# Kernel tuning notes

Measured on AMD Instinct MI355X. Metric: run time of the kernel, lower is better.

Reference implementation:

```python
import jax, jax.numpy as jnp
import numpy as np

B, N, DEG, F_IN, D = 32, 1024, 16, 8, 64

def setup_inputs() -> dict:
    key = jax.random.key(0)
    ks = jax.random.split(key, 24)
    T = B * N
    E = B * N * DEG
    x = jax.random.normal(ks[0], (T, F_IN), dtype=jnp.float32)
    # edges confined within each graph (block-diagonal batched graph)
    off = (jnp.arange(B) * N)[:, None]
    src = jax.random.randint(ks[1], (B, N * DEG), 0, N) + off
    dst = jax.random.randint(ks[2], (B, N * DEG), 0, N) + off
    edge_index = jnp.stack([src.reshape(-1), dst.reshape(-1)]).astype(jnp.int64)
    reachable = jax.random.randint(ks[3], (T,), 0, 2, dtype=jnp.int32)
    s = 0.1
    p = lambda k, shp: jax.random.normal(k, shp, dtype=jnp.float32) * s
    return {
        'x': x, 'edge_index': edge_index, 'reachable': reachable,
        'Wl0': p(ks[4], (D, F_IN)), 'Wr0': p(ks[5], (D, F_IN)),
        'att0': p(ks[6], (D,)), 'b0': p(ks[7], (D,)),
        'Wl': p(ks[8], (4, D, D)), 'Wr': p(ks[9], (4, D, D)),
        'att': p(ks[10], (4, D)), 'b': p(ks[11], (4, D)),
        't6w': p(ks[12], (D, D)), 't6b': p(ks[13], (D,)),
        't7w': p(ks[14], (D, D)), 't7b': p(ks[15], (D,)),
        't5pw': p(ks[16], (1, 2 * D)), 't5pb': p(ks[17], (1,)),
        't5vw': p(ks[18], (1, 2 * D)), 't5vb': p(ks[19], (1,)),
        'pw': p(ks[20], (1, 1)), 'pb': p(ks[21], (1,)),
        'vw': p(ks[22], (1, 1)), 'vb': p(ks[23], (1,)),
        'n_per_graph': N,
    }

def reference(x, edge_index, reachable, Wl0, Wr0, att0, b0, Wl, Wr, att, b,
              t6w, t6b, t7w, t7b, t5pw, t5pb, t5vw, t5vb, pw, pb, vw, vb,
              n_per_graph):
    T = x.shape[0]
    n = int(n_per_graph)
    bsz = T // n
    d = Wl0.shape[0]
    # GATv2Conv adds self loops by default
    loop = jnp.arange(T)
    src = jnp.concatenate([edge_index[0], loop])
    dst = jnp.concatenate([edge_index[1], loop])

    def gatv2(h, WlK, WrK, a, bb):
        xl = h @ WlK.T                                  # [T, d]
        xr = h @ WrK.T
        e = jax.nn.leaky_relu(xl[src] + xr[dst], 0.2) @ a  # [E]
        emax = jax.ops.segment_max(e, dst, num_segments=T)
        ee = jnp.exp(e - emax[dst])
        denom = jax.ops.segment_sum(ee, dst, num_segments=T)
        alpha = ee / denom[dst]                         # edge softmax per target
        return jax.ops.segment_sum(alpha[:, None] * xl[src], dst, num_segments=T) + bb

    h = gatv2(x, Wl0, Wr0, att0, b0)
    for k in range(Wl.shape[0]):  # ReLU between layers, none after last
        h = gatv2(jax.nn.relu(h), Wl[k], Wr[k], att[k], b[k])
    mu_raw = h                                          # [T, d]

    # scatter_mean pooling per graph + repeat_interleave back to nodes
    mu_mp = mu_raw.reshape(bsz, n, d).mean(axis=1)      # [B, d]
    mu_mp_exp = jnp.repeat(mu_mp, n, axis=0)            # [T, d]

    g = mu_mp_exp @ t6w.T + t6b
    l = mu_raw @ t7w.T + t7b
    rep = jax.nn.relu(jnp.concatenate([g, l], axis=1))  # [T, 2d]

    prob_logits = rep @ t5pw.T + t5pb                   # [T, 1]
    logits = (prob_logits * pw[0, 0] + pb[0]).reshape(bsz, n, 1)

    q = (rep @ t5vw.T + t5vb)[:, 0]                     # [T]
    q = jnp.where(reachable.astype(bool), q, jnp.float32(-1e20))
    v = q.reshape(bsz, n).max(axis=1, keepdims=True)    # [B, 1]
    value = v * vw[0, 0] + vb[0]
    return logits, value
```

## Files before the change

kernel.cpp:

```cpp
#include <hip/hip_runtime.h>
#include <hip/hip_bf16.h>

typedef unsigned short u16;

#define T_NODES 32768
#define NPG 1024
#define BGR 32
#define D 64
#define FIN 8
#define SLOTS 64

typedef __attribute__((ext_vector_type(8))) short short8v;
typedef __attribute__((ext_vector_type(4))) float floatx4;
typedef __attribute__((ext_vector_type(2))) float f32x2;

__device__ __forceinline__ float bf2f(u16 u){ return __uint_as_float(((unsigned)u) << 16); }
__device__ __forceinline__ u16 f2bf(float f){
    __hip_bfloat16 h = __float2bfloat16(f);
    return *reinterpret_cast<u16*>(&h);
}
__device__ __forceinline__ f32x2 lo_hi(unsigned w){
    f32x2 r;
    r[0] = __uint_as_float(w << 16);
    r[1] = __uint_as_float(w & 0xffff0000u);
    return r;
}
__device__ __forceinline__ f32x2 lrelu2(f32x2 v){
    return __builtin_elementwise_max(v, v * 0.2f);
}
__device__ __forceinline__ short8v pack_bf8(float4 a, float4 b){
    short8v r;
    r[0]=(short)f2bf(a.x); r[1]=(short)f2bf(a.y);
    r[2]=(short)f2bf(a.z); r[3]=(short)f2bf(a.w);
    r[4]=(short)f2bf(b.x); r[5]=(short)f2bf(b.y);
    r[6]=(short)f2bf(b.z); r[7]=(short)f2bf(b.w);
    return r;
}

__device__ __forceinline__ unsigned fenc(float f){
    unsigned b = __float_as_uint(f);
    return (b & 0x80000000u) ? ~b : (b | 0x80000000u);
}
__device__ __forceinline__ float fdec(unsigned k){
    unsigned b = (k & 0x80000000u) ? (k ^ 0x80000000u) : ~k;
    return __uint_as_float(b);
}

template<int CTRL, int RM, int BM>
__device__ __forceinline__ float dpp_add(float x){
    int y = __builtin_amdgcn_update_dpp(0, __float_as_int(x), CTRL, RM, BM, false);
    return x + __int_as_float(y);
}
__device__ __forceinline__ float wave_sum63(float x){
    x = dpp_add<0x111,0xf,0xf>(x);
    x = dpp_add<0x112,0xf,0xf>(x);
    x = dpp_add<0x114,0xf,0xe>(x);
    x = dpp_add<0x118,0xf,0xc>(x);
    x = dpp_add<0x142,0xa,0xf>(x);
    x = dpp_add<0x143,0xc,0xf>(x);
    return x;
}
__device__ __forceinline__ float wave_sum_bcast(float x){
    return __int_as_float(__builtin_amdgcn_readlane(__float_as_int(wave_sum63(x)), 63));
}
__device__ __forceinline__ float row_ror_add(float x){
    x = dpp_add<0x121,0xf,0xf>(x);
    x = dpp_add<0x122,0xf,0xf>(x);
    x = dpp_add<0x124,0xf,0xf>(x);
    x = dpp_add<0x128,0xf,0xf>(x);
    return x;
}

__device__ __forceinline__ void edge_body(uint2 uv, bool valid,
        f32x2 a01, f32x2 a23, f32x2 xr01, f32x2 xr23,
        f32x2& acc01, f32x2& acc23, float& l){
    f32x2 x01 = lo_hi(uv.x);
    f32x2 x23 = lo_hi(uv.y);
    f32x2 v01 = lrelu2(x01 + xr01);
    f32x2 v23 = lrelu2(x23 + xr23);
    f32x2 e2 = v01 * a01 + v23 * a23;
    float e = e2[0] + e2[1];
    e = row_ror_add(e);
    float q = valid ? __expf(e) : 0.f;
    acc01 += q * x01;
    acc23 += q * x23;
    l += q;
}

__device__ __forceinline__ void node_edge(const u16* __restrict__ xlin,
        const int* colSh, int eb, int t, int deg, int sub4,
        f32x2 a01, f32x2 a23, f32x2 xr01, f32x2 xr23,
        f32x2& acc01, f32x2& acc23, float& l){
    int nEdge = deg + 1;
    for (int j0 = 0; j0 < nEdge; j0 += 8){
        uint2 u[8];
        #pragma unroll
        for (int i = 0; i < 8; i++){
            int j = j0 + i;
            int jc = (j < nEdge) ? j : (nEdge-1);
            int s = (jc < deg) ? colSh[eb + jc] : t;
            u[i] = *(const uint2*)&xlin[((size_t)(unsigned)s << 6) + sub4];
        }
        #pragma unroll
        for (int i = 0; i < 8; i++)
            edge_body(u[i], j0 + i < nEdge, a01, a23, xr01, xr23, acc01, acc23, l);
    }
}

__device__ __forceinline__ void el_phase(
        const u16* __restrict__ xlin, const u16* __restrict__ xrin,
        const float* __restrict__ att, const float* __restrict__ bias,
        const float* __restrict__ Wl, const float* __restrict__ Wr,
        u16* __restrict__ xlout, u16* __restrict__ xrout,
        int tid, int rowBase, u16 (*hs)[80], const int* colSh, const int* cnt){
    int wave = tid >> 6, lane = tid & 63;
    int g = lane >> 4, sub4 = (lane & 15) << 2;
    int ln = wave*4 + g;
    int t  = rowBase + ln;
    f32x2 a01 = { att[sub4],   att[sub4+1] };
    f32x2 a23 = { att[sub4+2], att[sub4+3] };
    float4 b4 = *(const float4*)&bias[sub4];
    uint2 xru = *(const uint2*)&xrin[((size_t)t << 6) + sub4];
    f32x2 xr01 = lo_hi(xru.x), xr23 = lo_hi(xru.y);
    int deg = cnt[ln]; deg = deg < SLOTS ? deg : SLOTS;
    f32x2 acc01 = {0.f,0.f}, acc23 = {0.f,0.f};
    float l = 0.f;
    node_edge(xlin, colSh, ln*SLOTS, t, deg, sub4,
              a01, a23, xr01, xr23, acc01, acc23, l);
    float rl = __frcp_rn(l);
    ushort4 hb;
    hb.x = f2bf(fmaxf(fmaf(acc01[0], rl, b4.x), 0.f));
    hb.y = f2bf(fmaxf(fmaf(acc01[1], rl, b4.y), 0.f));
    hb.z = f2bf(fmaxf(fmaf(acc23[0], rl, b4.z), 0.f));
    hb.w = f2bf(fmaxf(fmaf(acc23[1], rl, b4.w), 0.f));
    *(ushort4*)&hs[ln][sub4] = hb;
    int lw = lane & 15, lg = lane >> 4, kb = lg*8;
    int colw = (wave << 4) + lw;
    const float* wl0 = &Wl[colw*D + kb];
    const float* wr0 = &Wr[colw*D + kb];
    short8v bl0 = pack_bf8(*(const float4*)wl0,        *(const float4*)(wl0+4));
    short8v bl1 = pack_bf8(*(const float4*)(wl0+32),   *(const float4*)(wl0+36));
    short8v br0 = pack_bf8(*(const float4*)wr0,        *(const float4*)(wr0+4));
    short8v br1 = pack_bf8(*(const float4*)(wr0+32),   *(const float4*)(wr0+36));
    __syncthreads();
    short8v a0 = *(const short8v*)&hs[lw][kb];
    short8v a1 = *(const short8v*)&hs[lw][32 + kb];
    floatx4 cl = {0.f,0.f,0.f,0.f}, cr = {0.f,0.f,0.f,0.f};
    cl = __builtin_amdgcn_mfma_f32_16x16x32_bf16(a0, bl0, cl, 0, 0, 0);
    cl = __builtin_amdgcn_mfma_f32_16x16x32_bf16(a1, bl1, cl, 0, 0, 0);
    cr = __builtin_amdgcn_mfma_f32_16x16x32_bf16(a0, br0, cr, 0, 0, 0);
    cr = __builtin_amdgcn_mfma_f32_16x16x32_bf16(a1, br1, cr, 0, 0, 0);
    size_t rb = (size_t)(rowBase + lg*4);
    #pragma unroll
    for (int j = 0; j < 4; j++){
        xlout[(rb + j)*D + colw] = f2bf(cl[j]);
        xrout[(rb + j)*D + colw] = f2bf(cr[j]);
    }
}

__global__ void lin0_kernel(const float* __restrict__ x, const float* __restrict__ Wl0,
                            const float* __restrict__ Wr0,
                            u16* __restrict__ xlb, u16* __restrict__ xrb,
                            float* __restrict__ muAcc,
                            unsigned* __restrict__ vslot, int* __restrict__ done,
                            int* __restrict__ pgdone, int* __restrict__ pgflag){
    __shared__ float wl[D][FIN+1];
    __shared__ float wr[D][FIN+1];
    __shared__ float xs[32][FIN];
    int tid = threadIdx.x;
    int blk = blockIdx.x;
    int gidx = blk*256 + tid;
    if (gidx < BGR*D)   muAcc[gidx] = 0.f;
    if (gidx < BGR){ vslot[gidx] = 0u; done[gidx] = 0; pgdone[gidx] = 0; pgflag[gidx] = 0; }
    int rowBase = (blk & 7)*4096 + (blk >> 3)*32;
    for (int i = tid; i < D*FIN; i += 256){
        wl[i>>3][i&7] = Wl0[i];
        wr[i>>3][i&7] = Wr0[i];
    }
    xs[tid>>3][tid&7] = x[rowBase*FIN + tid];
    __syncthreads();
    int wave = tid >> 6, lane = tid & 63;
    int rb = rowBase + wave*8;
    #pragma unroll
    for (int r = 0; r < 8; r++){
        float al = 0.f, ar = 0.f;
        int lr = wave*8 + r;
        #pragma unroll
        for (int k = 0; k < FIN; k++){
            float xv = xs[lr][k];
            al = fmaf(xv, wl[lane][k], al);
            ar = fmaf(xv, wr[lane][k], ar);
        }
        xlb[(size_t)(rb+r)*D + lane] = f2bf(al);
        xrb[(size_t)(rb+r)*D + lane] = f2bf(ar);
    }
}

__global__ __launch_bounds__(256) void el0_kernel(
        const int* __restrict__ esrc, const int* __restrict__ edst, int epg,
        const u16* __restrict__ xlin, const u16* __restrict__ xrin,
        const float* __restrict__ att, const float* __restrict__ bias,
        int* __restrict__ counts, int* __restrict__ col64,
        const float* __restrict__ Wl, const float* __restrict__ Wr,
        u16* __restrict__ xlout, u16* __restrict__ xrout){
    __shared__ __align__(16) u16 hs[16][80];
    __shared__ __align__(16) int colSh[16*SLOTS];
    __shared__ int cntL[16];
    int tid = threadIdx.x, blk = blockIdx.x;
    int rowBase = (blk & 7)*4096 + (blk >> 3)*16;
    int g = rowBase >> 10;
    if (tid < 16) cntL[tid] = 0;
    __syncthreads();
    size_t eg0 = (size_t)g * epg;
    const int4* d4 = (const int4*)(edst + eg0);
    const int4* s4 = (const int4*)(esrc + eg0);
    int q4 = epg >> 2;
    for (int i = tid; i < q4; i += 256){
        int4 dv = d4[i];
        int4 sv = s4[i];
        int r;
        r = dv.x - rowBase; if ((unsigned)r < 16u){ int sl = atomicAdd(&cntL[r], 1); if (sl < SLOTS) colSh[(r<<6)+sl] = sv.x; }
        r = dv.y - rowBase; if ((unsigned)r < 16u){ int sl = atomicAdd(&cntL[r], 1); if (sl < SLOTS) colSh[(r<<6)+sl] = sv.y; }
        r = dv.z - rowBase; if ((unsigned)r < 16u){ int sl = atomicAdd(&cntL[r], 1); if (sl < SLOTS) colSh[(r<<6)+sl] = sv.z; }
        r = dv.w - rowBase; if ((unsigned)r < 16u){ int sl = atomicAdd(&cntL[r], 1); if (sl < SLOTS) colSh[(r<<6)+sl] = sv.w; }
    }
    __syncthreads();
    if (tid < 16) counts[rowBase + tid] = cntL[tid];
    *(int4*)&col64[((size_t)rowBase << 6) + tid*4] = *(const int4*)&colSh[tid*4];
    el_phase(xlin, xrin, att, bias, Wl, Wr, xlout, xrout,
             tid, rowBase, hs, colSh, cntL);
}

__global__ __launch_bounds__(256) void el_kernel(
        const u16* __restrict__ xlin, const u16* __restrict__ xrin,
        const float* __restrict__ att, const float* __restrict__ bias,
        const int* __restrict__ counts, const int* __restrict__ col64,
        const float* __restrict__ Wl, const float* __restrict__ Wr,
        u16* __restrict__ xlout, u16* __restrict__ xrout){
    __shared__ __align__(16) u16 hs[16][80];
    __shared__ __align__(16) int colSh[16*SLOTS];
    __shared__ int cnt[16];
    int tid = threadIdx.x, blk = blockIdx.x;
    int rowBase = (blk & 7)*4096 + (blk >> 3)*16;
    if (tid < 16) cnt[tid] = counts[rowBase + tid];
    *(int4*)&colSh[tid*4] = *(const int4*)&col64[((size_t)rowBase << 6) + tid*4];
    __syncthreads();
    el_phase(xlin, xrin, att, bias, Wl, Wr, xlout, xrout,
             tid, rowBase, hs, colSh, cnt);
}

__global__ __launch_bounds__(256) void e4final_kernel(
        const u16* __restrict__ xlin, const u16* __restrict__ xrin,
        const float* __restrict__ att, const float* __restrict__ bias,
        const int* __restrict__ counts, const int* __restrict__ col64,
        const float* __restrict__ t6w, const float* __restrict__ t6b,
        const float* __restrict__ t7w, const float* __restrict__ t7b,
        const float* __restrict__ t5pw, const float* __restrict__ t5pb,
        const float* __restrict__ t5vw, const float* __restrict__ t5vb,
        const float* __restrict__ pw, const float* __restrict__ pb,
        const float* __restrict__ vw, const float* __restrict__ vb,
        const int* __restrict__ reachable,
        float* __restrict__ muAcc, unsigned* __restrict__ vslot,
        int* __restrict__ done, int* __restrict__ pgdone,
        int* __restrict__ pgflag, float* __restrict__ gPQ,
        float* __restrict__ out_logits, float* __restrict__ out_value){
    __shared__ __align__(16) char arena[43776];
    __shared__ float muS[D];
    __shared__ float PgQgS[2];
    __shared__ int isLastS;
    float* hfin  = (float*)arena;
    int*   colSh = (int*)  (arena + 17408);
    int*   cnt   = (int*)  (arena + 33792);
    float* wsH   = (float*)(arena + 17408);
    float* ppar  = (float*)(arena + 34816);
    float* qpar  = (float*)(arena + 39168);

    int tid = threadIdx.x, blk = blockIdx.x;
    int rowBase = (blk & 7)*4096 + (blk >> 3)*64;
    int b = rowBase >> 10;
    if (tid < 64){
        int c = counts[rowBase + tid];
        cnt[tid] = c < SLOTS ? c : SLOTS;
    }
    for (int i = tid; i < 1024; i += 256)
        *(int4*)&colSh[i*4] = *(const int4*)&col64[((size_t)rowBase << 6) + i*4];
    __syncthreads();
    int wave = tid >> 6, lane = tid & 63;
    int g = lane >> 4, sub4 = (lane & 15) << 2;
    int gid = wave*4 + g;
    f32x2 a01 = { att[sub4],   att[sub4+1] };
    f32x2 a23 = { att[sub4+2], att[sub4+3] };
    float4 b4 = *(const float4*)&bias[sub4];
    for (int n = 0; n < 4; n++){
        int ln = gid + n*16;
        int t  = rowBase + ln;
        uint2 xru = *(const uint2*)&xrin[((size_t)t << 6) + sub4];
        f32x2 xr01 = lo_hi(xru.x), xr23 = lo_hi(xru.y);
        int deg = cnt[ln];
        f32x2 acc01 = {0.f,0.f}, acc23 = {0.f,0.f};
        float l = 0.f;
        node_edge(xlin, colSh, ln*SLOTS, t, deg, sub4,
                  a01, a23, xr01, xr23, acc01, acc23, l);
        float rl = __frcp_rn(l);
        float4 hv;
        hv.x = fmaf(acc01[0], rl, b4.x);
        hv.y = fmaf(acc01[1], rl, b4.y);
        hv.z = fmaf(acc23[0], rl, b4.z);
        hv.w = fmaf(acc23[1], rl, b4.w);
        *(float4*)&hfin[ln*68 + sub4] = hv;
    }
    __syncthreads();
    for (int i = tid; i < D*D; i += 256) wsH[(i>>6)*68 + (i&63)] = t7w[i];
    if (wave == 0){
        float s = 0.f;
        #pragma unroll
        for (int nn = 0; nn < 64; nn++) s += hfin[nn*68 + lane];
        atomicAdd(&muAcc[b*D + lane], s);
    }
    __syncthreads();
    if (tid == 0){
        int tk = atomicAdd(&pgdone[b], 1);
        isLastS = (tk == (NPG/64) - 1);
    }
    __syncthreads();
    if (isLastS){
        if (tid < D)
            muS[tid] = __hip_atomic_load(&muAcc[b*D + tid], __ATOMIC_RELAXED,
                                         __HIP_MEMORY_SCOPE_AGENT) * (1.f/NPG);
        __syncthreads();
        if (tid < D){
            int d = tid;
            float gg = t6b[d];
            #pragma unroll
            for (int k = 0; k < D; k++) gg = fmaf(muS[k], t6w[d*D + k], gg);
            gg = fmaxf(gg, 0.f);
            float pp = wave_sum_bcast(gg * t5pw[d]);
            float qq = wave_sum_bcast(gg * t5vw[d]);
            if (d == 0){
                __hip_atomic_store(&gPQ[b*2],   pp, __ATOMIC_RELAXED, __HIP_MEMORY_SCOPE_AGENT);
                __hip_atomic_store(&gPQ[b*2+1], qq, __ATOMIC_RELAXED, __HIP_MEMORY_SCOPE_AGENT);
                asm volatile("s_waitcnt vmcnt(0)" ::: "memory");
                __hip_atomic_store(&pgflag[b], 1, __ATOMIC_RELAXED, __HIP_MEMORY_SCOPE_AGENT);
            }
        }
    }
    int ty = tid >> 4, tx = tid & 15;
    int r0 = ty * 4;
    float acc[4][4];
    #pragma unroll
    for (int i = 0; i < 4; i++)
        #pragma unroll
        for (int j = 0; j < 4; j++) acc[i][j] = 0.f;
    for (int k = 0; k < D; k += 4){
        float4 hv[4], wv[4];
        #pragma unroll
        for (int i = 0; i < 4; i++){
            hv[i] = *(const float4*)&hfin[(r0+i)*68 + k];
            wv[i] = *(const float4*)&wsH[(tx + 16*i)*68 + k];
        }
        #pragma unroll
        for (int i = 0; i < 4; i++)
            #pragma unroll
            for (int j = 0; j < 4; j++)
                acc[i][j] += hv[i].x*wv[j].x + hv[i].y*wv[j].y
                           + hv[i].z*wv[j].z + hv[i].w*wv[j].w;
    }
    float bc[4], pwc[4], qwc[4];
    #pragma unroll
    for (int j = 0; j < 4; j++){
        int c = tx + 16*j;
        bc[j]  = t7b[c];
        pwc[j] = t5pw[D + c];
        qwc[j] = t5vw[D + c];
    }
    #pragma unroll
    for (int i = 0; i < 4; i++){
        float sp = 0.f, sq = 0.f;
        #pragma unroll
        for (int j = 0; j < 4; j++){
            float lv = fmaxf(acc[i][j] + bc[j], 0.f);
            sp = fmaf(lv, pwc[j], sp);
            sq = fmaf(lv, qwc[j], sq);
        }
        ppar[(r0+i)*17 + tx] = sp;
        qpar[(r0+i)*17 + tx] = sq;
    }
    __syncthreads();
    if (tid == 0){
        while (__hip_atomic_load(&pgflag[b], __ATOMIC_RELAXED,
                                 __HIP_MEMORY_SCOPE_AGENT) == 0)
            __builtin_amdgcn_s_sleep(16);
        PgQgS[0] = __hip_atomic_load(&gPQ[b*2],   __ATOMIC_RELAXED, __HIP_MEMORY_SCOPE_AGENT);
        PgQgS[1] = __hip_atomic_load(&gPQ[b*2+1], __ATOMIC_RELAXED, __HIP_MEMORY_SCOPE_AGENT);
    }
    __syncthreads();
    if (tid < 64){
        int t = rowBase + tid;
        float sp = 0.f, sq = 0.f;
        #pragma unroll
        for (int c = 0; c < 16; c++){ sp += ppar[tid*17 + c]; sq += qpar[tid*17 + c]; }
        float prob = PgQgS[0] + sp + t5pb[0];
        out_logits[t] = prob * pw[0] + pb[0];
        float q = PgQgS[1] + sq + t5vb[0];
        if (!reachable[t]) q = -1e20f;
        float m = q;
        #pragma unroll
        for (int o = 1; o < 64; o <<= 1) m = fmaxf(m, __shfl_xor(m, o, 64));
        if (tid == 0){
            atomicMax(&vslot[b], fenc(m));
            asm volatile("s_waitcnt vmcnt(0)" ::: "memory");
            int ticket = atomicAdd(&done[b], 1);
            if (ticket == (NPG/64) - 1){
                unsigned k = __hip_atomic_load(&vslot[b], __ATOMIC_RELAXED,
                                               __HIP_MEMORY_SCOPE_AGENT);
                out_value[b] = fdec(k)*vw[0] + vb[0];
            }
        }
    }
}

extern "C" void kernel_launch(void* const* d_in, const int* in_sizes, int n_in,
                              void* d_out, int out_size, void* d_ws, size_t ws_size,
                              hipStream_t stream){
    const float* x          = (const float*)d_in[0];
    const int*   edge_index = (const int*)d_in[1];
    const int*   reachable  = (const int*)d_in[2];
    const float* Wl0 = (const float*)d_in[3];
    const float* Wr0 = (const float*)d_in[4];
    const float* att0= (const float*)d_in[5];
    const float* b0  = (const float*)d_in[6];
    const float* Wl  = (const float*)d_in[7];
    const float* Wr  = (const float*)d_in[8];
    const float* att = (const float*)d_in[9];
    const float* bb  = (const float*)d_in[10];
    const float* t6w = (const float*)d_in[11];
    const float* t6b = (const float*)d_in[12];
    const float* t7w = (const float*)d_in[13];
    const float* t7b = (const float*)d_in[14];
    const float* t5pw= (const float*)d_in[15];
    const float* t5pb= (const float*)d_in[16];
    const float* t5vw= (const float*)d_in[17];
    const float* t5vb= (const float*)d_in[18];
    const float* pw  = (const float*)d_in[19];
    const float* pb  = (const float*)d_in[20];
    const float* vw  = (const float*)d_in[21];
    const float* vb  = (const float*)d_in[22];

    int E = in_sizes[1] / 2;
    int epg = E / BGR;
    const int* esrc = edge_index;
    const int* edst = edge_index + E;

    char* ws = (char*)d_ws;
    u16* xlbA   = (u16*)ws;
    u16* xrbA   = xlbA + (size_t)T_NODES*D;
    u16* xlbB   = xrbA + (size_t)T_NODES*D;
    u16* xrbB   = xlbB + (size_t)T_NODES*D;
    int* counts = (int*)(xrbB + (size_t)T_NODES*D);
    int* col64  = counts + T_NODES + 16;
    float* muAcc= (float*)(col64 + (size_t)T_NODES*SLOTS);
    unsigned* vslot = (unsigned*)(muAcc + BGR*D);
    int* done   = (int*)(vslot + BGR);
    int* pgdone = done + BGR;
    int* pgflag = pgdone + BGR;
    float* gPQ  = (float*)(pgflag + BGR);

    lin0_kernel<<<T_NODES/32, 256, 0, stream>>>(x, Wl0, Wr0, xlbA, xrbA,
                                                muAcc, vslot, done, pgdone, pgflag);

    el0_kernel<<<T_NODES/16, 256, 0, stream>>>(esrc, edst, epg, xlbA, xrbA, att0, b0,
                                               counts, col64,
                                               Wl + 0*D*D, Wr + 0*D*D, xlbB, xrbB);
    el_kernel<<<T_NODES/16, 256, 0, stream>>>(xlbB, xrbB, att + 0*D, bb + 0*D, counts, col64,
                                              Wl + 1*D*D, Wr + 1*D*D, xlbA, xrbA);
    el_kernel<<<T_NODES/16, 256, 0, stream>>>(xlbA, xrbA, att + 1*D, bb + 1*D, counts, col64,
                                              Wl + 2*D*D, Wr + 2*D*D, xlbB, xrbB);
    el_kernel<<<T_NODES/16, 256, 0, stream>>>(xlbB, xrbB, att + 2*D, bb + 2*D, counts, col64,
                                              Wl + 3*D*D, Wr + 3*D*D, xlbA, xrbA);

    e4final_kernel<<<T_NODES/64, 256, 0, stream>>>(xlbA, xrbA, att + 3*D, bb + 3*D,
                                                   counts, col64, t6w, t6b, t7w, t7b,
                                                   t5pw, t5pb, t5vw, t5vb, pw, pb, vw, vb,
                                                   reachable, muAcc, vslot, done,
                                                   pgdone, pgflag, gPQ,
                                                   (float*)d_out, (float*)d_out + T_NODES);
}
```

Before: 223.3 us.

## Compress adjacency to 16-bit local indices, pre-convert weights, fuse xr0 into el0

Neighbor lists are now stored as u16 offsets relative to the graph base instead of 32-bit global ids, halving adjacency traffic in every layer. The per-layer weights are converted to bf16 once in lin0 instead of being packed from fp32 in every block. The first layer's xr projection is computed on the fly inside el0 from x and Wr0 rather than written and re-read from global memory. This relies on graphs having at most 65536 nodes and adds some redundant small FMA work in el0.

```diff
diff --git a/kernel.cpp b/kernel.cpp
--- a/kernel.cpp
+++ b/kernel.cpp
@@ -27,14 +27,6 @@
 }
 __device__ __forceinline__ f32x2 lrelu2(f32x2 v){
     return __builtin_elementwise_max(v, v * 0.2f);
-}
-__device__ __forceinline__ short8v pack_bf8(float4 a, float4 b){
-    short8v r;
-    r[0]=(short)f2bf(a.x); r[1]=(short)f2bf(a.y);
-    r[2]=(short)f2bf(a.z); r[3]=(short)f2bf(a.w);
-    r[4]=(short)f2bf(b.x); r[5]=(short)f2bf(b.y);
-    r[6]=(short)f2bf(b.z); r[7]=(short)f2bf(b.w);
-    return r;
 }
 
 __device__ __forceinline__ unsigned fenc(float f){
@@ -88,7 +80,7 @@
 }
 
 __device__ __forceinline__ void node_edge(const u16* __restrict__ xlin,
-        const int* colSh, int eb, int t, int deg, int sub4,
+        const u16* colSh, int eb, int gbase, int t, int deg, int sub4,
         f32x2 a01, f32x2 a23, f32x2 xr01, f32x2 xr23,
         f32x2& acc01, f32x2& acc23, float& l){
     int nEdge = deg + 1;
@@ -98,7 +90,7 @@
         for (int i = 0; i < 8; i++){
             int j = j0 + i;
             int jc = (j < nEdge) ? j : (nEdge-1);
-            int s = (jc < deg) ? colSh[eb + jc] : t;
+            int s = (jc < deg) ? (gbase + (int)colSh[eb + jc]) : t;
             u[i] = *(const uint2*)&xlin[((size_t)(unsigned)s << 6) + sub4];
         }
         #pragma unroll
@@ -108,24 +100,24 @@
 }
 
 __device__ __forceinline__ void el_phase(
-        const u16* __restrict__ xlin, const u16* __restrict__ xrin,
+        const u16* __restrict__ xlin,
         const float* __restrict__ att, const float* __restrict__ bias,
-        const float* __restrict__ Wl, const float* __restrict__ Wr,
+        const u16* __restrict__ Wlb, const u16* __restrict__ Wrb,
         u16* __restrict__ xlout, u16* __restrict__ xrout,
-        int tid, int rowBase, u16 (*hs)[80], const int* colSh, const int* cnt){
+        int tid, int rowBase, u16 (*hs)[80], const u16* colSh, const int* cnt,
+        f32x2 xr01, f32x2 xr23){
     int wave = tid >> 6, lane = tid & 63;
     int g = lane >> 4, sub4 = (lane & 15) << 2;
     int ln = wave*4 + g;
     int t  = rowBase + ln;
+    int gbase = (rowBase >> 10) << 10;
     f32x2 a01 = { att[sub4],   att[sub4+1] };
     f32x2 a23 = { att[sub4+2], att[sub4+3] };
     float4 b4 = *(const float4*)&bias[sub4];
-    uint2 xru = *(const uint2*)&xrin[((size_t)t << 6) + sub4];
-    f32x2 xr01 = lo_hi(xru.x), xr23 = lo_hi(xru.y);
     int deg = cnt[ln]; deg = deg < SLOTS ? deg : SLOTS;
     f32x2 acc01 = {0.f,0.f}, acc23 = {0.f,0.f};
     float l = 0.f;
-    node_edge(xlin, colSh, ln*SLOTS, t, deg, sub4,
+    node_edge(xlin, colSh, ln*SLOTS, gbase, t, deg, sub4,
               a01, a23, xr01, xr23, acc01, acc23, l);
     float rl = __frcp_rn(l);
     ushort4 hb;
@@ -136,12 +128,12 @@
     *(ushort4*)&hs[ln][sub4] = hb;
     int lw = lane & 15, lg = lane >> 4, kb = lg*8;
     int colw = (wave << 4) + lw;
-    const float* wl0 = &Wl[colw*D + kb];
-    const float* wr0 = &Wr[colw*D + kb];
-    short8v bl0 = pack_bf8(*(const float4*)wl0,        *(const float4*)(wl0+4));
-    short8v bl1 = pack_bf8(*(const float4*)(wl0+32),   *(const float4*)(wl0+36));
-    short8v br0 = pack_bf8(*(const float4*)wr0,        *(const float4*)(wr0+4));
-    short8v br1 = pack_bf8(*(const float4*)(wr0+32),   *(const float4*)(wr0+36));
+    const u16* wlp = &Wlb[colw*D + kb];
+    const u16* wrp = &Wrb[colw*D + kb];
+    short8v bl0 = *(const short8v*)wlp;
+    short8v bl1 = *(const short8v*)(wlp + 32);
+    short8v br0 = *(const short8v*)wrp;
+    short8v br1 = *(const short8v*)(wrp + 32);
     __syncthreads();
     short8v a0 = *(const short8v*)&hs[lw][kb];
     short8v a1 = *(const short8v*)&hs[lw][32 + kb];
@@ -159,59 +151,67 @@
 }
 
 __global__ void lin0_kernel(const float* __restrict__ x, const float* __restrict__ Wl0,
-                            const float* __restrict__ Wr0,
-                            u16* __restrict__ xlb, u16* __restrict__ xrb,
+                            const float* __restrict__ Wl, const float* __restrict__ Wr,
+                            u16* __restrict__ xlb,
+                            u16* __restrict__ Wlb, u16* __restrict__ Wrb,
                             float* __restrict__ muAcc,
                             unsigned* __restrict__ vslot, int* __restrict__ done,
                             int* __restrict__ pgdone, int* __restrict__ pgflag){
     __shared__ float wl[D][FIN+1];
-    __shared__ float wr[D][FIN+1];
     __shared__ float xs[32][FIN];
     int tid = threadIdx.x;
     int blk = blockIdx.x;
     int gidx = blk*256 + tid;
     if (gidx < BGR*D)   muAcc[gidx] = 0.f;
     if (gidx < BGR){ vslot[gidx] = 0u; done[gidx] = 0; pgdone[gidx] = 0; pgflag[gidx] = 0; }
+    if (gidx < 4*D*D){
+        Wlb[gidx] = f2bf(Wl[gidx]);
+        Wrb[gidx] = f2bf(Wr[gidx]);
+    }
     int rowBase = (blk & 7)*4096 + (blk >> 3)*32;
-    for (int i = tid; i < D*FIN; i += 256){
+    for (int i = tid; i < D*FIN; i += 256)
         wl[i>>3][i&7] = Wl0[i];
-        wr[i>>3][i&7] = Wr0[i];
-    }
     xs[tid>>3][tid&7] = x[rowBase*FIN + tid];
     __syncthreads();
     int wave = tid >> 6, lane = tid & 63;
     int rb = rowBase + wave*8;
     #pragma unroll
     for (int r = 0; r < 8; r++){
-        float al = 0.f, ar = 0.f;
+        float al = 0.f;
         int lr = wave*8 + r;
         #pragma unroll
-        for (int k = 0; k < FIN; k++){
-            float xv = xs[lr][k];
-            al = fmaf(xv, wl[lane][k], al);
-            ar = fmaf(xv, wr[lane][k], ar);
-        }
+        for (int k = 0; k < FIN; k++)
+            al = fmaf(xs[lr][k], wl[lane][k], al);
         xlb[(size_t)(rb+r)*D + lane] = f2bf(al);
-        xrb[(size_t)(rb+r)*D + lane] = f2bf(ar);
     }
 }
 
 __global__ __launch_bounds__(256) void el0_kernel(
         const int* __restrict__ esrc, const int* __restrict__ edst, int epg,
-        const u16* __restrict__ xlin, const u16* __restrict__ xrin,
+        const float* __restrict__ x, const float* __restrict__ Wr0,
+        const u16* __restrict__ xlin,
         const float* __restrict__ att, const float* __restrict__ bias,
-        int* __restrict__ counts, int* __restrict__ col64,
-        const float* __restrict__ Wl, const float* __restrict__ Wr,
+        int* __restrict__ counts, u16* __restrict__ col64u,
+        const u16* __restrict__ Wlb, const u16* __restrict__ Wrb,
         u16* __restrict__ xlout, u16* __restrict__ xrout){
     __shared__ __align__(16) u16 hs[16][80];
-    __shared__ __align__(16) int colSh[16*SLOTS];
+    __shared__ __align__(16) u16 colSh[16*SLOTS];
     __shared__ int cntL[16];
+    __shared__ float xsS[16][FIN];
+    __shared__ float wrT[FIN][D];
     int tid = threadIdx.x, blk = blockIdx.x;
     int rowBase = (blk & 7)*4096 + (blk >> 3)*16;
-    int g = rowBase >> 10;
+    int gg = rowBase >> 10;
+    int gbase = gg << 10;
     if (tid < 16) cntL[tid] = 0;
-    __syncthreads();
-    size_t eg0 = (size_t)g * epg;
+    if (tid < 128) xsS[tid>>3][tid&7] = x[(rowBase + (tid>>3))*FIN + (tid&7)];
+    #pragma unroll
+    for (int it = 0; it < 2; it++){
+        int i = it*256 + tid;
+        wrT[i&7][i>>3] = Wr0[i];
+    }
+    __syncthreads();
+    size_t eg0 = (size_t)gg * epg;
     const int4* d4 = (const int4*)(edst + eg0);
     const int4* s4 = (const int4*)(esrc + eg0);
     int q4 = epg >> 2;
@@ -219,40 +219,60 @@
         int4 dv = d4[i];
         int4 sv = s4[i];
         int r;
-        r = dv.x - rowBase; if ((unsigned)r < 16u){ int sl = atomicAdd(&cntL[r], 1); if (sl < SLOTS) colSh[(r<<6)+sl] = sv.x; }
-        r = dv.y - rowBase; if ((unsigned)r < 16u){ int sl = atomicAdd(&cntL[r], 1); if (sl < SLOTS) colSh[(r<<6)+sl] = sv.y; }
-        r = dv.z - rowBase; if ((unsigned)r < 16u){ int sl = atomicAdd(&cntL[r], 1); if (sl < SLOTS) colSh[(r<<6)+sl] = sv.z; }
-        r = dv.w - rowBase; if ((unsigned)r < 16u){ int sl = atomicAdd(&cntL[r], 1); if (sl < SLOTS) colSh[(r<<6)+sl] = sv.w; }
+        r = dv.x - rowBase; if ((unsigned)r < 16u){ int sl = atomicAdd(&cntL[r], 1); if (sl < SLOTS) colSh[(r<<6)+sl] = (u16)(sv.x - gbase); }
+        r = dv.y - rowBase; if ((unsigned)r < 16u){ int sl = atomicAdd(&cntL[r], 1); if (sl < SLOTS) colSh[(r<<6)+sl] = (u16)(sv.y - gbase); }
+        r = dv.z - rowBase; if ((unsigned)r < 16u){ int sl = atomicAdd(&cntL[r], 1); if (sl < SLOTS) colSh[(r<<6)+sl] = (u16)(sv.z - gbase); }
+        r = dv.w - rowBase; if ((unsigned)r < 16u){ int sl = atomicAdd(&cntL[r], 1); if (sl < SLOTS) colSh[(r<<6)+sl] = (u16)(sv.w - gbase); }
     }
     __syncthreads();
     if (tid < 16) counts[rowBase + tid] = cntL[tid];
-    *(int4*)&col64[((size_t)rowBase << 6) + tid*4] = *(const int4*)&colSh[tid*4];
-    el_phase(xlin, xrin, att, bias, Wl, Wr, xlout, xrout,
-             tid, rowBase, hs, colSh, cntL);
+    *(int2*)&col64u[(size_t)rowBase*SLOTS + tid*4] = *(const int2*)&colSh[tid*4];
+    int wave = tid >> 6, lane = tid & 63;
+    int g = lane >> 4, sub4 = (lane & 15) << 2;
+    int ln = wave*4 + g;
+    float4 xr4 = make_float4(0.f,0.f,0.f,0.f);
+    #pragma unroll
+    for (int k = 0; k < FIN; k++){
+        float xv = xsS[ln][k];
+        float4 w4 = *(const float4*)&wrT[k][sub4];
+        xr4.x = fmaf(xv, w4.x, xr4.x);
+        xr4.y = fmaf(xv, w4.y, xr4.y);
+        xr4.z = fmaf(xv, w4.z, xr4.z);
+        xr4.w = fmaf(xv, w4.w, xr4.w);
+    }
+    f32x2 xr01 = { xr4.x, xr4.y }, xr23 = { xr4.z, xr4.w };
+    el_phase(xlin, att, bias, Wlb, Wrb, xlout, xrout,
+             tid, rowBase, hs, colSh, cntL, xr01, xr23);
 }
 
 __global__ __launch_bounds__(256) void el_kernel(
         const u16* __restrict__ xlin, const u16* __restrict__ xrin,
         const float* __restrict__ att, const float* __restrict__ bias,
-        const int* __restrict__ counts, const int* __restrict__ col64,
-        const float* __restrict__ Wl, const float* __restrict__ Wr,
+        const int* __restrict__ counts, const u16* __restrict__ col64u,
+        const u16* __restrict__ Wlb, const u16* __restrict__ Wrb,
         u16* __restrict__ xlout, u16* __restrict__ xrout){
     __shared__ __align__(16) u16 hs[16][80];
-    __shared__ __align__(16) int colSh[16*SLOTS];
+    __shared__ __align__(16) u16 colSh[16*SLOTS];
     __shared__ int cnt[16];
     int tid = threadIdx.x, blk = blockIdx.x;
     int rowBase = (blk & 7)*4096 + (blk >> 3)*16;
     if (tid < 16) cnt[tid] = counts[rowBase + tid];
-    *(int4*)&colSh[tid*4] = *(const int4*)&col64[((size_t)rowBase << 6) + tid*4];
-    __syncthreads();
-    el_phase(xlin, xrin, att, bias, Wl, Wr, xlout, xrout,
-             tid, rowBase, hs, colSh, cnt);
+    *(int2*)&colSh[tid*4] = *(const int2*)&col64u[(size_t)rowBase*SLOTS + tid*4];
+    __syncthreads();
+    int wave = tid >> 6, lane = tid & 63;
+    int g = lane >> 4, sub4 = (lane & 15) << 2;
+    int ln = wave*4 + g;
+    int t  = rowBase + ln;
+    uint2 xru = *(const uint2*)&xrin[((size_t)t << 6) + sub4];
+    f32x2 xr01 = lo_hi(xru.x), xr23 = lo_hi(xru.y);
+    el_phase(xlin, att, bias, Wlb, Wrb, xlout, xrout,
+             tid, rowBase, hs, colSh, cnt, xr01, xr23);
 }
 
 __global__ __launch_bounds__(256) void e4final_kernel(
         const u16* __restrict__ xlin, const u16* __restrict__ xrin,
         const float* __restrict__ att, const float* __restrict__ bias,
-        const int* __restrict__ counts, const int* __restrict__ col64,
+        const int* __restrict__ counts, const u16* __restrict__ col64u,
         const float* __restrict__ t6w, const float* __restrict__ t6b,
         const float* __restrict__ t7w, const float* __restrict__ t7b,
         const float* __restrict__ t5pw, const float* __restrict__ t5pb,
@@ -269,8 +289,8 @@
     __shared__ float PgQgS[2];
     __shared__ int isLastS;
     float* hfin  = (float*)arena;
-    int*   colSh = (int*)  (arena + 17408);
-    int*   cnt   = (int*)  (arena + 33792);
+    u16*   colSh = (u16*)  (arena + 17408);
+    int*   cnt   = (int*)  (arena + 25600);
     float* wsH   = (float*)(arena + 17408);
     float* ppar  = (float*)(arena + 34816);
     float* qpar  = (float*)(arena + 39168);
@@ -278,12 +298,16 @@
     int tid = threadIdx.x, blk = blockIdx.x;
     int rowBase = (blk & 7)*4096 + (blk >> 3)*64;
     int b = rowBase >> 10;
+    int gbase = b << 10;
     if (tid < 64){
         int c = counts[rowBase + tid];
         cnt[tid] = c < SLOTS ? c : SLOTS;
     }
-    for (int i = tid; i < 1024; i += 256)
-        *(int4*)&colSh[i*4] = *(const int4*)&col64[((size_t)rowBase << 6) + i*4];
+    #pragma unroll
+    for (int it = 0; it < 2; it++){
+        int i = it*256 + tid;
+        *(int4*)&colSh[i*8] = *(const int4*)&col64u[(size_t)rowBase*SLOTS + i*8];
+    }
     __syncthreads();
     int wave = tid >> 6, lane = tid & 63;
     int g = lane >> 4, sub4 = (lane & 15) << 2;
@@ -299,7 +323,7 @@
         int deg = cnt[ln];
         f32x2 acc01 = {0.f,0.f}, acc23 = {0.f,0.f};
         float l = 0.f;
-        node_edge(xlin, colSh, ln*SLOTS, t, deg, sub4,
+        node_edge(xlin, colSh, ln*SLOTS, gbase, t, deg, sub4,
                   a01, a23, xr01, xr23, acc01, acc23, l);
         float rl = __frcp_rn(l);
         float4 hv;
@@ -330,12 +354,12 @@
         __syncthreads();
         if (tid < D){
             int d = tid;
-            float gg = t6b[d];
+            float gv = t6b[d];
             #pragma unroll
-            for (int k = 0; k < D; k++) gg = fmaf(muS[k], t6w[d*D + k], gg);
-            gg = fmaxf(gg, 0.f);
-            float pp = wave_sum_bcast(gg * t5pw[d]);
-            float qq = wave_sum_bcast(gg * t5vw[d]);
+            for (int k = 0; k < D; k++) gv = fmaf(muS[k], t6w[d*D + k], gv);
+            gv = fmaxf(gv, 0.f);
+            float pp = wave_sum_bcast(gv * t5pw[d]);
+            float qq = wave_sum_bcast(gv * t5vw[d]);
             if (d == 0){
                 __hip_atomic_store(&gPQ[b*2],   pp, __ATOMIC_RELAXED, __HIP_MEMORY_SCOPE_AGENT);
                 __hip_atomic_store(&gPQ[b*2+1], qq, __ATOMIC_RELAXED, __HIP_MEMORY_SCOPE_AGENT);
@@ -457,29 +481,31 @@
     u16* xlbB   = xrbA + (size_t)T_NODES*D;
     u16* xrbB   = xlbB + (size_t)T_NODES*D;
     int* counts = (int*)(xrbB + (size_t)T_NODES*D);
-    int* col64  = counts + T_NODES + 16;
-    float* muAcc= (float*)(col64 + (size_t)T_NODES*SLOTS);
+    u16* col64u = (u16*)(counts + T_NODES + 16);
+    float* muAcc= (float*)(col64u + (size_t)T_NODES*SLOTS);
     unsigned* vslot = (unsigned*)(muAcc + BGR*D);
     int* done   = (int*)(vslot + BGR);
     int* pgdone = done + BGR;
     int* pgflag = pgdone + BGR;
     float* gPQ  = (float*)(pgflag + BGR);
-
-    lin0_kernel<<<T_NODES/32, 256, 0, stream>>>(x, Wl0, Wr0, xlbA, xrbA,
+    u16* Wlb    = (u16*)(gPQ + 2*BGR);
+    u16* Wrb    = Wlb + 4*D*D;
+
+    lin0_kernel<<<T_NODES/32, 256, 0, stream>>>(x, Wl0, Wl, Wr, xlbA, Wlb, Wrb,
                                                 muAcc, vslot, done, pgdone, pgflag);
 
-    el0_kernel<<<T_NODES/16, 256, 0, stream>>>(esrc, edst, epg, xlbA, xrbA, att0, b0,
-                                               counts, col64,
-                                               Wl + 0*D*D, Wr + 0*D*D, xlbB, xrbB);
-    el_kernel<<<T_NODES/16, 256, 0, stream>>>(xlbB, xrbB, att + 0*D, bb + 0*D, counts, col64,
-                                              Wl + 1*D*D, Wr + 1*D*D, xlbA, xrbA);
-    el_kernel<<<T_NODES/16, 256, 0, stream>>>(xlbA, xrbA, att + 1*D, bb + 1*D, counts, col64,
-                                              Wl + 2*D*D, Wr + 2*D*D, xlbB, xrbB);
-    el_kernel<<<T_NODES/16, 256, 0, stream>>>(xlbB, xrbB, att + 2*D, bb + 2*D, counts, col64,
-                                              Wl + 3*D*D, Wr + 3*D*D, xlbA, xrbA);
+    el0_kernel<<<T_NODES/16, 256, 0, stream>>>(esrc, edst, epg, x, Wr0, xlbA, att0, b0,
+                                               counts, col64u, Wlb + 0*D*D, Wrb + 0*D*D,
+                                               xlbB, xrbB);
+    el_kernel<<<T_NODES/16, 256, 0, stream>>>(xlbB, xrbB, att + 0*D, bb + 0*D, counts, col64u,
+                                              Wlb + 1*D*D, Wrb + 1*D*D, xlbA, xrbA);
+    el_kernel<<<T_NODES/16, 256, 0, stream>>>(xlbA, xrbA, att + 1*D, bb + 1*D, counts, col64u,
+                                              Wlb + 2*D*D, Wrb + 2*D*D, xlbB, xrbB);
+    el_kernel<<<T_NODES/16, 256, 0, stream>>>(xlbB, xrbB, att + 2*D, bb + 2*D, counts, col64u,
+                                              Wlb + 3*D*D, Wrb + 3*D*D, xlbA, xrbA);
 
     e4final_kernel<<<T_NODES/64, 256, 0, stream>>>(xlbA, xrbA, att + 3*D, bb + 3*D,
-                                                   counts, col64, t6w, t6b, t7w, t7b,
+                                                   counts, col64u, t6w, t6b, t7w, t7b,
                                                    t5pw, t5pb, t5vw, t5vb, pw, pb, vw, vb,
                                                    reachable, muAcc, vslot, done,
                                                    pgdone, pgflag, gPQ,
```

Result: no change. 225.1 us (+0.8%).
